# Kernel tuning notes

Hardware: AMD Instinct MI355X
Metric: run time of the kernel (lower is better)

The kernel has to match this reference:

```python
import jax, jax.numpy as jnp
import numpy as np

B, V, E = 1024, 50257, 128

def setup_inputs() -> dict:
    key = jax.random.key(0)
    k1, k2, k3, k4 = jax.random.split(key, 4)
    # xs: one-hot focus-word vectors [B, V]
    focus_ids = jax.random.randint(k1, (B,), 0, V)
    xs = jnp.zeros((B, V), dtype=jnp.float32).at[jnp.arange(B), focus_ids].set(1.0)
    metric = jax.random.normal(k2, (E, E), dtype=jnp.float32)
    EMBEDM = jax.random.normal(k3, (V, E), dtype=jnp.float32)
    NEGEMBEDM = jax.random.normal(k4, (V, E), dtype=jnp.float32)
    return {"xs": xs, "metric": metric, "EMBEDM": EMBEDM, "NEGEMBEDM": NEGEMBEDM}

def reference(xs, metric, EMBEDM, NEGEMBEDM):
    # xs @ EMBEDM : one-hot matmul == row gather, but kept as GEMM to match original math
    xsembeds = xs @ EMBEDM                              # [B, E]
    # dots(vs, ws, metric) = (vs @ metric) @ ws.T
    scores = (xsembeds @ metric) @ NEGEMBEDM.T          # [B, V]
    return jax.nn.log_softmax(scores, axis=1)
```

## Files before the change

kernel.cpp:

```cpp
#include <hip/hip_runtime.h>
#include <hip/hip_bf16.h>
#include <math.h>

#define B_ROWS 1024
#define V_COLS 50257
#define E_DIM  128
#define BM     128
#define BN     128
#define NNB    393
#define VPAD   (NNB * BN)
#define N4     (V_COLS * E_DIM / 4)
#define N4P    (VPAD * E_DIM / 4)
#define NCHUNK 32

typedef __attribute__((ext_vector_type(8))) short short8;
typedef __attribute__((ext_vector_type(4))) float floatx4;

static __device__ __forceinline__ unsigned short f2bf(float x) {
    union { float f; unsigned int u; } c; c.f = x;
    unsigned int u = c.u;
    unsigned int r = u + 0x7fffu + ((u >> 16) & 1u);
    return (unsigned short)(r >> 16);
}

static __device__ __forceinline__ void gload16(const void* g, void* l) {
    __builtin_amdgcn_global_load_lds(
        (const __attribute__((address_space(1))) void*)g,
        (__attribute__((address_space(3))) void*)l,
        16, 0, 0);
}

__global__ void find_idx_kernel(const float* __restrict__ xs, int* __restrict__ idx) {
    long i = (long)blockIdx.x * blockDim.x + threadIdx.x;
    const long n4 = (long)B_ROWS * V_COLS / 4;
    if (i >= n4) return;
    floatx4 v = __builtin_nontemporal_load((const floatx4*)xs + i);
    float vals[4] = {v.x, v.y, v.z, v.w};
    #pragma unroll
    for (int c = 0; c < 4; ++c) {
        if (vals[c] != 0.0f) {
            long f = 4 * i + c;
            int b = (int)(f / V_COLS);
            idx[b] = (int)(f - (long)b * V_COLS);
        }
    }
}

__global__ void cvt_bf16_kernel(const float* __restrict__ src, ushort4* __restrict__ dst) {
    int i = blockIdx.x * blockDim.x + threadIdx.x;
    if (i >= N4P) return;
    ushort4 o;
    if (i < N4) {
        floatx4 v = __builtin_nontemporal_load((const floatx4*)src + i);
        o.x = f2bf(v.x); o.y = f2bf(v.y); o.z = f2bf(v.z); o.w = f2bf(v.w);
    } else {
        o.x = 0; o.y = 0; o.z = 0; o.w = 0;
    }
    dst[i] = o;
}

__global__ void compute_t_kernel(const float* __restrict__ EMB, const float* __restrict__ metric,
                                 const int* __restrict__ idx, unsigned short* __restrict__ t) {
    __shared__ float erow[E_DIM];
    int b = blockIdx.x, tid = threadIdx.x;
    int id = idx[b];
    erow[tid] = EMB[(long)id * E_DIM + tid];
    __syncthreads();
    float acc = 0.f;
    #pragma unroll 16
    for (int k = 0; k < E_DIM; ++k) acc += erow[k] * metric[k * E_DIM + tid];
    t[b * E_DIM + tid] = f2bf(acc);
}

template <bool WRITE_OUT>
__global__ __launch_bounds__(512, 2) void gemm_chunk_kernel(const unsigned short* __restrict__ t,
                                                            const unsigned short* __restrict__ neg,
                                                            float2* __restrict__ partials,
                                                            const float* __restrict__ lse,
                                                            float* __restrict__ out) {
    __shared__ __align__(16) uint4 bbuf[2][2048];

    const int lin  = blockIdx.x;
    const int m    = (lin >> 3) & 7;
    const int c    = (lin & 7) | ((lin >> 6) << 3);
    const int t0   = (c * NNB) / NCHUNK;
    const int t1   = ((c + 1) * NNB) / NCHUNK;

    const int tid  = threadIdx.x;
    const int lane = tid & 63, wave = tid >> 6;
    const int l16  = lane & 15, q = lane >> 4;
    const int wm   = wave >> 2, wn = wave & 3;
    const int mbase = m * BM;

    short8 af[4][4];
    #pragma unroll
    for (int mf = 0; mf < 4; ++mf)
        #pragma unroll
        for (int ks = 0; ks < 4; ++ks)
            af[mf][ks] = *(const short8*)&t[(size_t)(mbase + wm * 64 + mf * 16 + l16) * E_DIM + ks * 32 + q * 8];

    float lsev[4][4];
    float mrun[4][4], srun[4][4];
    if (WRITE_OUT) {
        #pragma unroll
        for (int mf = 0; mf < 4; ++mf)
            #pragma unroll
            for (int r = 0; r < 4; ++r)
                lsev[mf][r] = lse[mbase + wm * 64 + mf * 16 + q * 4 + r];
    } else {
        #pragma unroll
        for (int mf = 0; mf < 4; ++mf)
            #pragma unroll
            for (int r = 0; r < 4; ++r) { mrun[mf][r] = -INFINITY; srun[mf][r] = 0.f; }
    }

    const int p0 = wave * 256 + lane;
    auto STAGE = [&](int buf, int tile) {
        const uint4* srcB = (const uint4*)(neg + (size_t)tile * BN * E_DIM);
        #pragma unroll
        for (int i = 0; i < 4; ++i) {
            int p = p0 + i * 64;
            int r = p >> 4, cc = p & 15;
            int s = (r << 4) + (cc ^ (r & 15));
            gload16(srcB + s, &bbuf[buf][wave * 256 + i * 64]);
        }
    };

    STAGE(0, t0);
    __syncthreads();

    for (int tt = t0; tt < t1; ++tt) {
        const int cur = (tt - t0) & 1;
        if (tt + 1 < t1) STAGE(cur ^ 1, tt + 1);

        floatx4 acc[4][2];
        #pragma unroll
        for (int i = 0; i < 4; ++i)
            #pragma unroll
            for (int j = 0; j < 2; ++j) acc[i][j] = (floatx4){0, 0, 0, 0};

        #pragma unroll
        for (int ks = 0; ks < 4; ++ks) {
            short8 bfr[2];
            #pragma unroll
            for (int nf = 0; nf < 2; ++nf) {
                int row = wn * 32 + nf * 16 + l16;
                bfr[nf] = *(const short8*)&bbuf[cur][(row << 4) + ((ks * 4 + q) ^ (row & 15))];
            }
            #pragma unroll
            for (int mf = 0; mf < 4; ++mf)
                #pragma unroll
                for (int nf = 0; nf < 2; ++nf)
                    acc[mf][nf] = __builtin_amdgcn_mfma_f32_16x16x32_bf16(af[mf][ks], bfr[nf], acc[mf][nf], 0, 0, 0);
        }

        const int col0 = tt * BN + wn * 32 + l16;
        const bool v0 = col0 < V_COLS;
        const bool v1 = (col0 + 16) < V_COLS;

        if (!WRITE_OUT) {
            #pragma unroll
            for (int mf = 0; mf < 4; ++mf)
                #pragma unroll
                for (int r = 0; r < 4; ++r) {
                    float a0 = v0 ? acc[mf][0][r] : -INFINITY;
                    float a1 = v1 ? acc[mf][1][r] : -INFINITY;
                    float nm = fmaxf(mrun[mf][r], fmaxf(a0, a1));
                    float s  = srun[mf][r] * __expf(mrun[mf][r] - nm);
                    if (v0) s += __expf(a0 - nm);
                    if (v1) s += __expf(a1 - nm);
                    mrun[mf][r] = nm; srun[mf][r] = s;
                }
        } else {
            #pragma unroll
            for (int mf = 0; mf < 4; ++mf) {
                const size_t rowb = (size_t)(mbase + wm * 64 + mf * 16 + q * 4) * V_COLS;
                #pragma unroll
                for (int r = 0; r < 4; ++r) {
                    if (v0) out[rowb + (size_t)r * V_COLS + col0]      = acc[mf][0][r] - lsev[mf][r];
                    if (v1) out[rowb + (size_t)r * V_COLS + col0 + 16] = acc[mf][1][r] - lsev[mf][r];
                }
            }
        }
        __syncthreads();
    }

    if (!WRITE_OUT) {
        #pragma unroll
        for (int mf = 0; mf < 4; ++mf)
            #pragma unroll
            for (int r = 0; r < 4; ++r) {
                float mm = mrun[mf][r], ss = srun[mf][r];
                #pragma unroll
                for (int d = 1; d < 16; d <<= 1) {
                    float mo = __shfl_xor(mm, d, 16);
                    float so = __shfl_xor(ss, d, 16);
                    float nm = fmaxf(mm, mo);
                    ss = ss * __expf(mm - nm) + so * __expf(mo - nm);
                    mm = nm;
                }
                if (l16 == 0) {
                    int row_local = wm * 64 + mf * 16 + q * 4 + r;
                    partials[(((size_t)mbase + row_local) * NCHUNK + c) * 4 + wn] = make_float2(mm, ss);
                }
            }
    }
}

__global__ __launch_bounds__(128) void merge_lse_kernel(const float2* __restrict__ partials,
                                                        float* __restrict__ lse) {
    int b = blockIdx.x, tid = threadIdx.x;
    float2 p = partials[(size_t)b * 128 + tid];
    float mm = p.x, ss = p.y;
    #pragma unroll
    for (int d = 1; d < 64; d <<= 1) {
        float mo = __shfl_xor(mm, d, 64);
        float so = __shfl_xor(ss, d, 64);
        float nm = fmaxf(mm, mo);
        ss = ss * __expf(mm - nm) + so * __expf(mo - nm);
        mm = nm;
    }
    __shared__ float m2[2], s2[2];
    if ((tid & 63) == 0) { m2[tid >> 6] = mm; s2[tid >> 6] = ss; }
    __syncthreads();
    if (tid == 0) {
        float nm = fmaxf(m2[0], m2[1]);
        float s  = s2[0] * __expf(m2[0] - nm) + s2[1] * __expf(m2[1] - nm);
        lse[b] = nm + __logf(s);
    }
}

extern "C" void kernel_launch(void* const* d_in, const int* in_sizes, int n_in,
                              void* d_out, int out_size, void* d_ws, size_t ws_size,
                              hipStream_t stream) {
    const float* xs     = (const float*)d_in[0];
    const float* metric = (const float*)d_in[1];
    const float* EMB    = (const float*)d_in[2];
    const float* NEG    = (const float*)d_in[3];
    float* out = (float*)d_out;

    char* ws = (char*)d_ws;
    int*            idx      = (int*)ws;
    unsigned short* t        = (unsigned short*)(ws + 4096);
    unsigned short* neg16    = (unsigned short*)(ws + 266240);
    float2*         partials = (float2*)(ws + 13144064);
    float*          lse      = (float*)(ws + 14192640);

    {
        long n4 = (long)B_ROWS * V_COLS / 4;
        int blocks = (int)((n4 + 255) / 256);
        find_idx_kernel<<<blocks, 256, 0, stream>>>(xs, idx);
    }
    cvt_bf16_kernel<<<(N4P + 255) / 256, 256, 0, stream>>>(NEG, (ushort4*)neg16);
    compute_t_kernel<<<B_ROWS, E_DIM, 0, stream>>>(EMB, metric, idx, t);
    gemm_chunk_kernel<false><<<8 * NCHUNK, 512, 0, stream>>>(t, neg16, partials, nullptr, nullptr);
    merge_lse_kernel<<<B_ROWS, 128, 0, stream>>>(partials, lse);
    gemm_chunk_kernel<true><<<8 * NCHUNK, 512, 0, stream>>>(t, neg16, partials, lse, out);
}
```

Baseline: 438.5 us.

## Replace LDS-staged block GEMM with independent per-wave register-pipelined tiles

Each wave now owns a 64-row group and a contiguous chunk of 32-column steps. It loads the bf16 NEGEMBEDM fragments straight from global memory into registers with double buffering, with no LDS staging and no block-level __syncthreads. The grid grows to 2048 waves across 128 column chunks, and the partials layout is simplified to match. The aim is to remove barrier and LDS overhead and to add parallelism. In exchange, B-tile reuse across waves in a block is lost, so each B row is fetched by 16 row groups and L2 traffic rises.

```diff
diff --git a/kernel.cpp b/kernel.cpp
--- a/kernel.cpp
+++ b/kernel.cpp
@@ -5,13 +5,12 @@
 #define B_ROWS 1024
 #define V_COLS 50257
 #define E_DIM  128
-#define BM     128
-#define BN     128
-#define NNB    393
-#define VPAD   (NNB * BN)
+#define VPAD   50304
+#define NNB4   (VPAD / 4)
 #define N4     (V_COLS * E_DIM / 4)
 #define N4P    (VPAD * E_DIM / 4)
-#define NCHUNK 32
+#define NSTEPS (VPAD / 32)
+#define NCH    128
 
 typedef __attribute__((ext_vector_type(8))) short short8;
 typedef __attribute__((ext_vector_type(4))) float floatx4;
@@ -21,13 +20,6 @@
     unsigned int u = c.u;
     unsigned int r = u + 0x7fffu + ((u >> 16) & 1u);
     return (unsigned short)(r >> 16);
-}
-
-static __device__ __forceinline__ void gload16(const void* g, void* l) {
-    __builtin_amdgcn_global_load_lds(
-        (const __attribute__((address_space(1))) void*)g,
-        (__attribute__((address_space(3))) void*)l,
-        16, 0, 0);
 }
 
 __global__ void find_idx_kernel(const float* __restrict__ xs, int* __restrict__ idx) {
@@ -73,40 +65,34 @@
 }
 
 template <bool WRITE_OUT>
-__global__ __launch_bounds__(512, 2) void gemm_chunk_kernel(const unsigned short* __restrict__ t,
-                                                            const unsigned short* __restrict__ neg,
-                                                            float2* __restrict__ partials,
-                                                            const float* __restrict__ lse,
-                                                            float* __restrict__ out) {
-    __shared__ __align__(16) uint4 bbuf[2][2048];
-
-    const int lin  = blockIdx.x;
-    const int m    = (lin >> 3) & 7;
-    const int c    = (lin & 7) | ((lin >> 6) << 3);
-    const int t0   = (c * NNB) / NCHUNK;
-    const int t1   = ((c + 1) * NNB) / NCHUNK;
-
-    const int tid  = threadIdx.x;
-    const int lane = tid & 63, wave = tid >> 6;
+__global__ __launch_bounds__(256, 2) void gemm_wave_kernel(const unsigned short* __restrict__ t,
+                                                           const unsigned short* __restrict__ neg,
+                                                           float2* __restrict__ partials,
+                                                           const float* __restrict__ lse,
+                                                           float* __restrict__ out) {
+    const int wave = threadIdx.x >> 6, lane = threadIdx.x & 63;
     const int l16  = lane & 15, q = lane >> 4;
-    const int wm   = wave >> 2, wn = wave & 3;
-    const int mbase = m * BM;
+    const int gw   = blockIdx.x * 4 + wave;
+    const int rowgrp = gw & 15;
+    const int chunk  = gw >> 4;
+    const int s0 = (chunk * NSTEPS) / NCH;
+    const int s1 = ((chunk + 1) * NSTEPS) / NCH;
+    const int rowbase = rowgrp * 64;
 
     short8 af[4][4];
     #pragma unroll
     for (int mf = 0; mf < 4; ++mf)
         #pragma unroll
         for (int ks = 0; ks < 4; ++ks)
-            af[mf][ks] = *(const short8*)&t[(size_t)(mbase + wm * 64 + mf * 16 + l16) * E_DIM + ks * 32 + q * 8];
-
-    float lsev[4][4];
-    float mrun[4][4], srun[4][4];
+            af[mf][ks] = *(const short8*)&t[(size_t)(rowbase + mf * 16 + l16) * E_DIM + ks * 32 + q * 8];
+
+    float mrun[4][4], srun[4][4], lsev[4][4];
     if (WRITE_OUT) {
         #pragma unroll
         for (int mf = 0; mf < 4; ++mf)
             #pragma unroll
             for (int r = 0; r < 4; ++r)
-                lsev[mf][r] = lse[mbase + wm * 64 + mf * 16 + q * 4 + r];
+                lsev[mf][r] = lse[rowbase + mf * 16 + q * 4 + r];
     } else {
         #pragma unroll
         for (int mf = 0; mf < 4; ++mf)
@@ -114,49 +100,32 @@
             for (int r = 0; r < 4; ++r) { mrun[mf][r] = -INFINITY; srun[mf][r] = 0.f; }
     }
 
-    const int p0 = wave * 256 + lane;
-    auto STAGE = [&](int buf, int tile) {
-        const uint4* srcB = (const uint4*)(neg + (size_t)tile * BN * E_DIM);
-        #pragma unroll
-        for (int i = 0; i < 4; ++i) {
-            int p = p0 + i * 64;
-            int r = p >> 4, cc = p & 15;
-            int s = (r << 4) + (cc ^ (r & 15));
-            gload16(srcB + s, &bbuf[buf][wave * 256 + i * 64]);
-        }
+    auto LOADB = [&](short8 (&bf)[8], int s) {
+        const int cb = s * 32;
+        #pragma unroll
+        for (int nf = 0; nf < 2; ++nf)
+            #pragma unroll
+            for (int ks = 0; ks < 4; ++ks)
+                bf[nf * 4 + ks] = *(const short8*)&neg[(size_t)(cb + nf * 16 + l16) * E_DIM + ks * 32 + q * 8];
     };
 
-    STAGE(0, t0);
-    __syncthreads();
-
-    for (int tt = t0; tt < t1; ++tt) {
-        const int cur = (tt - t0) & 1;
-        if (tt + 1 < t1) STAGE(cur ^ 1, tt + 1);
-
+    auto COMPUTE = [&](const short8 (&bf)[8], int s) {
         floatx4 acc[4][2];
         #pragma unroll
         for (int i = 0; i < 4; ++i)
             #pragma unroll
             for (int j = 0; j < 2; ++j) acc[i][j] = (floatx4){0, 0, 0, 0};
-
-        #pragma unroll
-        for (int ks = 0; ks < 4; ++ks) {
-            short8 bfr[2];
-            #pragma unroll
-            for (int nf = 0; nf < 2; ++nf) {
-                int row = wn * 32 + nf * 16 + l16;
-                bfr[nf] = *(const short8*)&bbuf[cur][(row << 4) + ((ks * 4 + q) ^ (row & 15))];
-            }
+        #pragma unroll
+        for (int ks = 0; ks < 4; ++ks)
             #pragma unroll
             for (int mf = 0; mf < 4; ++mf)
                 #pragma unroll
                 for (int nf = 0; nf < 2; ++nf)
-                    acc[mf][nf] = __builtin_amdgcn_mfma_f32_16x16x32_bf16(af[mf][ks], bfr[nf], acc[mf][nf], 0, 0, 0);
-        }
-
-        const int col0 = tt * BN + wn * 32 + l16;
-        const bool v0 = col0 < V_COLS;
-        const bool v1 = (col0 + 16) < V_COLS;
+                    acc[mf][nf] = __builtin_amdgcn_mfma_f32_16x16x32_bf16(af[mf][ks], bf[nf * 4 + ks], acc[mf][nf], 0, 0, 0);
+
+        const int cb = s * 32;
+        const bool v0 = (cb + l16) < V_COLS;
+        const bool v1 = (cb + 16 + l16) < V_COLS;
 
         if (!WRITE_OUT) {
             #pragma unroll
@@ -166,23 +135,34 @@
                     float a0 = v0 ? acc[mf][0][r] : -INFINITY;
                     float a1 = v1 ? acc[mf][1][r] : -INFINITY;
                     float nm = fmaxf(mrun[mf][r], fmaxf(a0, a1));
-                    float s  = srun[mf][r] * __expf(mrun[mf][r] - nm);
-                    if (v0) s += __expf(a0 - nm);
-                    if (v1) s += __expf(a1 - nm);
-                    mrun[mf][r] = nm; srun[mf][r] = s;
+                    float sx = srun[mf][r] * __expf(mrun[mf][r] - nm);
+                    if (v0) sx += __expf(a0 - nm);
+                    if (v1) sx += __expf(a1 - nm);
+                    mrun[mf][r] = nm; srun[mf][r] = sx;
                 }
         } else {
             #pragma unroll
             for (int mf = 0; mf < 4; ++mf) {
-                const size_t rowb = (size_t)(mbase + wm * 64 + mf * 16 + q * 4) * V_COLS;
+                const size_t rowb = (size_t)(rowbase + mf * 16 + q * 4) * V_COLS;
                 #pragma unroll
                 for (int r = 0; r < 4; ++r) {
-                    if (v0) out[rowb + (size_t)r * V_COLS + col0]      = acc[mf][0][r] - lsev[mf][r];
-                    if (v1) out[rowb + (size_t)r * V_COLS + col0 + 16] = acc[mf][1][r] - lsev[mf][r];
+                    if (v0) out[rowb + (size_t)r * V_COLS + cb + l16]      = acc[mf][0][r] - lsev[mf][r];
+                    if (v1) out[rowb + (size_t)r * V_COLS + cb + 16 + l16] = acc[mf][1][r] - lsev[mf][r];
                 }
             }
         }
-        __syncthreads();
+    };
+
+    short8 bA[8], bB[8];
+    LOADB(bA, s0);
+    int s = s0;
+    for (;;) {
+        if (s + 1 < s1) LOADB(bB, s + 1);
+        COMPUTE(bA, s);
+        if (++s >= s1) break;
+        if (s + 1 < s1) LOADB(bA, s + 1);
+        COMPUTE(bB, s);
+        if (++s >= s1) break;
     }
 
     if (!WRITE_OUT) {
@@ -199,10 +179,8 @@
                     ss = ss * __expf(mm - nm) + so * __expf(mo - nm);
                     mm = nm;
                 }
-                if (l16 == 0) {
-                    int row_local = wm * 64 + mf * 16 + q * 4 + r;
-                    partials[(((size_t)mbase + row_local) * NCHUNK + c) * 4 + wn] = make_float2(mm, ss);
-                }
+                if (l16 == 0)
+                    partials[(size_t)(rowbase + mf * 16 + q * 4 + r) * NCH + chunk] = make_float2(mm, ss);
             }
     }
 }
@@ -210,7 +188,7 @@
 __global__ __launch_bounds__(128) void merge_lse_kernel(const float2* __restrict__ partials,
                                                         float* __restrict__ lse) {
     int b = blockIdx.x, tid = threadIdx.x;
-    float2 p = partials[(size_t)b * 128 + tid];
+    float2 p = partials[(size_t)b * NCH + tid];
     float mm = p.x, ss = p.y;
     #pragma unroll
     for (int d = 1; d < 64; d <<= 1) {
@@ -253,7 +231,7 @@
     }
     cvt_bf16_kernel<<<(N4P + 255) / 256, 256, 0, stream>>>(NEG, (ushort4*)neg16);
     compute_t_kernel<<<B_ROWS, E_DIM, 0, stream>>>(EMB, metric, idx, t);
-    gemm_chunk_kernel<false><<<8 * NCHUNK, 512, 0, stream>>>(t, neg16, partials, nullptr, nullptr);
+    gemm_wave_kernel<false><<<512, 256, 0, stream>>>(t, neg16, partials, nullptr, nullptr);
     merge_lse_kernel<<<B_ROWS, 128, 0, stream>>>(partials, lse);
-    gemm_chunk_kernel<true><<<8 * NCHUNK, 512, 0, stream>>>(t, neg16, partials, lse, out);
-}
+    gemm_wave_kernel<true><<<512, 256, 0, stream>>>(t, neg16, partials, lse, out);
+}
```

Result: slower. 504.1 us (+15.0%).
